# Performance work log

Measured on AMD Instinct MI355X. Metric: run time of the kernel, lower is better.

## Reference

```python
import jax, jax.numpy as jnp
import numpy as np

L = 4          # num_layers
H = 512        # hidden_size == input_size
B, S = 8, 4096
LN_EPS = 1e-5


def parallel_scan_log(coeffs, values):
    """h_t = coeffs_t * h_{t-1} + values_t via Hillis-Steele log-step scan.
    coeffs, values: (B, S, H). Faithful to the torch loop incl. clamp."""
    seq_len = coeffs.shape[1]
    a = jnp.clip(coeffs, 1e-08, 1.0 - 1e-08)
    b = values
    num_steps = int(seq_len - 1).bit_length()
    for step in range(num_steps):
        d = 1 << step
        if d >= seq_len:
            break
        a_prev = jnp.pad(a[:, :-d, :], ((0, 0), (d, 0), (0, 0)), constant_values=1.0)
        b_prev = jnp.pad(b[:, :-d, :], ((0, 0), (d, 0), (0, 0)), constant_values=0.0)
        b = a * b_prev + b   # uses old a (matches a_new/b_new then assign)
        a = a * a_prev
    return b


def mingru_layer(x, Wz, bz, Wh, bh):
    # x: (B,S,in) ; Wz,Wh: (H,in) torch Linear layout (y = x @ W.T + b)
    z = jax.nn.sigmoid(jnp.einsum('bsi,hi->bsh', x, Wz) + bz)
    h_tilde = jnp.tanh(jnp.einsum('bsi,hi->bsh', x, Wh) + bh)
    return parallel_scan_log(1.0 - z, z * h_tilde)


def layer_norm(x, g, b):
    mu = jnp.mean(x, axis=-1, keepdims=True)
    var = jnp.mean(jnp.square(x - mu), axis=-1, keepdims=True)
    return (x - mu) * jax.lax.rsqrt(var + LN_EPS) * g + b


def run_layers(x, Wz, bz, Wh, bh, ln_g, ln_b):
    h = x
    for i in range(L):
        h_new = mingru_layer(h, Wz[i], bz[i], Wh[i], bh[i])
        if i > 0:
            h_new = h_new + h  # residual (shapes match for i>0)
        h = layer_norm(h_new, ln_g, ln_b)  # dropout==Identity (p=0)
    return h


def setup_inputs() -> dict:
    key = jax.random.key(0)
    ks = jax.random.split(key, 12)
    lim = 1.0 / np.sqrt(H)  # torch Linear default init range
    u = lambda k, shp: jax.random.uniform(k, shp, jnp.float32, -lim, lim)
    return {
        'x': jax.random.normal(ks[0], (B, S, H), jnp.float32),
        'Wz_f': u(ks[1], (L, H, H)), 'bz_f': u(ks[2], (L, H)),
        'Wh_f': u(ks[3], (L, H, H)), 'bh_f': u(ks[4], (L, H)),
        'Wz_b': u(ks[5], (L, H, H)), 'bz_b': u(ks[6], (L, H)),
        'Wh_b': u(ks[7], (L, H, H)), 'bh_b': u(ks[8], (L, H)),
        'fusion_w': u(ks[9], (H, 2 * H)), 'fusion_b': u(ks[10], (H,)),
        'ln_g': jnp.ones((H,), jnp.float32), 'ln_b': jnp.zeros((H,), jnp.float32),
    }


def reference(x, Wz_f, bz_f, Wh_f, bh_f, Wz_b, bz_b, Wh_b, bh_b, fusion_w, fusion_b, ln_g, ln_b):
    out_fwd = run_layers(x, Wz_f, bz_f, Wh_f, bh_f, ln_g, ln_b)
    x_rev = jnp.flip(x, axis=1)
    out_bwd = jnp.flip(run_layers(x_rev, Wz_b, bz_b, Wh_b, bh_b, ln_g, ln_b), axis=1)
    out_comb = jnp.concatenate([out_fwd, out_bwd], axis=-1)  # (B,S,2H)
    return jnp.einsum('bsk,hk->bsh', out_comb, fusion_w) + fusion_b
```

## Files before the change

### kernel.cpp

```cpp
#include <hip/hip_runtime.h>

#define HID 512
#define SLEN 4096
#define NB 8
#define BSROWS (NB*SLEN)
#define NLAYER 4
#define CHUNKT 128
#define NCHUNK 32

typedef float f32x4 __attribute__((ext_vector_type(4)));
typedef unsigned int u32x4 __attribute__((ext_vector_type(4)));

__device__ __forceinline__ float bf2f(unsigned short u){
  union { unsigned int i; float f; } v; v.i = ((unsigned int)u) << 16; return v.f;
}
__device__ __forceinline__ unsigned short f2bf(float f){
  union { float f; unsigned int i; } v; v.f = f;
  unsigned int u = v.i;
  u = u + 0x7fffu + ((u >> 16) & 1u);
  return (unsigned short)(u >> 16);
}
__device__ __forceinline__ void mfma_bf16(f32x4& acc, u32x4 a, u32x4 b){
  asm("v_mfma_f32_16x16x32_bf16 %0, %1, %2, %0" : "+v"(acc) : "v"(a), "v"(b));
}
__device__ __forceinline__ void mfma_fence(){
  __builtin_amdgcn_sched_barrier(0);
  asm volatile("s_nop 7\n\ts_nop 7\n\ts_nop 7\n\ts_nop 7");
  __builtin_amdgcn_sched_barrier(0);
}
__device__ __forceinline__ void decode_ab(unsigned int v, float& a, float& b){
  a = (float)(v & 0xffffu) * (1.f/65535.f);
  b = fmaf((float)(v >> 16), 2.f/65535.f, -1.f);
}


__global__ __launch_bounds__(256) void prep_w(
    const float* __restrict__ wzf, const float* __restrict__ whf,
    const float* __restrict__ wzb, const float* __restrict__ whb,
    unsigned short* __restrict__ wbf)
{
  int idx = blockIdx.x*256 + threadIdx.x;
  int i8  = idx & 63;
  int o   = (idx >> 6) & 511;
  int m   = (idx >> 15) & 1;
  int l   = (idx >> 16) & 3;
  int dir = idx >> 18;
  const float* src = dir ? (m ? whb : wzb) : (m ? whf : wzf);
  const float* p = src + ((size_t)(l*512 + o)*512 + i8*8);
  float4 v0 = *(const float4*)p;
  float4 v1 = *(const float4*)(p+4);
  unsigned short* q = wbf + ((((size_t)(dir*4 + l)*2 + m)*512 + o)*512 + i8*8);
  u32x4 outv;
  outv[0] = (unsigned)f2bf(v0.x) | ((unsigned)f2bf(v0.y)<<16);
  outv[1] = (unsigned)f2bf(v0.z) | ((unsigned)f2bf(v0.w)<<16);
  outv[2] = (unsigned)f2bf(v1.x) | ((unsigned)f2bf(v1.y)<<16);
  outv[3] = (unsigned)f2bf(v1.z) | ((unsigned)f2bf(v1.w)<<16);
  *(u32x4*)q = outv;
}

__global__ __launch_bounds__(256) void prep_fw(
    const float* __restrict__ fw, unsigned short* __restrict__ outw)
{
  int idx = blockIdx.x*256 + threadIdx.x;
  const float* p = fw + (size_t)idx*8;
  float4 v0 = *(const float4*)p;
  float4 v1 = *(const float4*)(p+4);
  u32x4 outv;
  outv[0] = (unsigned)f2bf(v0.x) | ((unsigned)f2bf(v0.y)<<16);
  outv[1] = (unsigned)f2bf(v0.z) | ((unsigned)f2bf(v0.w)<<16);
  outv[2] = (unsigned)f2bf(v1.x) | ((unsigned)f2bf(v1.y)<<16);
  outv[3] = (unsigned)f2bf(v1.z) | ((unsigned)f2bf(v1.w)<<16);
  *(u32x4*)(outw + (size_t)idx*8) = outv;
}

__global__ __launch_bounds__(256) void prep_x(
    const float* __restrict__ x, unsigned short* __restrict__ X0)
{
  int idx = blockIdx.x*256 + threadIdx.x;
  int j8  = idx & 63;
  int s   = (idx >> 6) & 4095;
  int b   = (idx >> 18) & 7;
  int dir = idx >> 21;
  int srcs = dir ? (4095 - s) : s;
  const float* p = x + ((size_t)(b*SLEN + srcs)*512 + j8*8);
  float4 v0 = *(const float4*)p;
  float4 v1 = *(const float4*)(p+4);
  u32x4 outv;
  outv[0] = (unsigned)f2bf(v0.x) | ((unsigned)f2bf(v0.y)<<16);
  outv[1] = (unsigned)f2bf(v0.z) | ((unsigned)f2bf(v0.w)<<16);
  outv[2] = (unsigned)f2bf(v1.x) | ((unsigned)f2bf(v1.y)<<16);
  outv[3] = (unsigned)f2bf(v1.z) | ((unsigned)f2bf(v1.w)<<16);
  *(u32x4*)(X0 + ((size_t)((dir*NB + b)*SLEN + s)*512 + j8*8)) = outv;
}


__global__ __launch_bounds__(256) void gate_gemm_scan(
    const unsigned short* __restrict__ X,
    const unsigned short* __restrict__ Wz,
    const unsigned short* __restrict__ Wh,
    const float* __restrict__ bzp, const float* __restrict__ bhp,
    unsigned int* __restrict__ PH,
    float* __restrict__ Aagg, float* __restrict__ Bagg,
    int Mtiles, int CG)
{
  __shared__ __align__(16) unsigned char smem[32768 + 2048];
  unsigned short* As  = (unsigned short*)smem;
  unsigned short* Bzs = (unsigned short*)(smem + 16384);
  unsigned short* Bhs = (unsigned short*)(smem + 24576);
  unsigned int*   SC  = (unsigned int*)smem;
  float* SegP = (float*)(smem + 32768);
  float* SegH = (float*)(smem + 32768 + 1024);

  int hw = blockIdx.x;
  int lg = (hw & 7)*Mtiles + (hw >> 3);
  int nt  = lg & 7;
  int mt  = lg >> 3;

  const int tid = threadIdx.x;
  const int lane = tid & 63;
  const int wv = tid >> 6;
  const int n0 = nt*64;
  const int slot = tid & 7;
  const int rowb = tid >> 3;

  f32x4 accz[2][4], acch[2][4];
  #pragma unroll
  for (int i=0;i<2;++i)
    #pragma unroll
    for (int j=0;j<4;++j){ accz[i][j] = (f32x4)(0.f); acch[i][j] = (f32x4)(0.f); }

  for (int ks=0; ks<8; ++ks){
    int k0 = ks*64;
    #pragma unroll
    for (int it=0; it<4; ++it){
      int row = rowb + it*32;
      u32x4 v = *(const u32x4*)(X + (size_t)(mt*128+row)*512 + k0 + slot*8);
      *(u32x4*)(As + row*64 + ((slot ^ (row&7))<<3)) = v;
    }
    #pragma unroll
    for (int it=0; it<2; ++it){
      int row = rowb + it*32;
      u32x4 vz = *(const u32x4*)(Wz + (size_t)(n0+row)*512 + k0 + slot*8);
      *(u32x4*)(Bzs + row*64 + ((slot ^ (row&7))<<3)) = vz;
      u32x4 vh = *(const u32x4*)(Wh + (size_t)(n0+row)*512 + k0 + slot*8);
      *(u32x4*)(Bhs + row*64 + ((slot ^ (row&7))<<3)) = vh;
    }
    __syncthreads();
    #pragma unroll
    for (int kk=0; kk<2; ++kk){
      int kslot = kk*4 + (lane >> 4);
      u32x4 af[2];
      #pragma unroll
      for (int mf=0; mf<2; ++mf){
        int row = wv*32 + mf*16 + (lane & 15);
        af[mf] = *(const u32x4*)(As + row*64 + ((kslot ^ (row&7))<<3));
      }
      #pragma unroll
      for (int nf=0; nf<4; ++nf){
        int row = nf*16 + (lane & 15);
        u32x4 bz = *(const u32x4*)(Bzs + row*64 + ((kslot ^ (row&7))<<3));
        u32x4 bh = *(const u32x4*)(Bhs + row*64 + ((kslot ^ (row&7))<<3));
        #pragma unroll
        for (int mf=0; mf<2; ++mf){
          mfma_bf16(accz[mf][nf], af[mf], bz);
          mfma_bf16(acch[mf][nf], af[mf], bh);
        }
      }
    }
    __syncthreads();
  }
  mfma_fence();

  #pragma unroll
  for (int nf=0; nf<4; ++nf){
    int colL = nf*16 + (lane & 15);
    float bz = bzp[n0 + colL];
    float bh = bhp[n0 + colL];
    #pragma unroll
    for (int mf=0; mf<2; ++mf){
      int rloc = wv*32 + mf*16 + ((lane>>4)<<2);
      #pragma unroll
      for (int r=0; r<4; ++r){
        float zp = accz[mf][nf][r] + bz;
        float hp = acch[mf][nf][r] + bh;
        float sg = 1.f/(1.f + __expf(-zp));
        float th = 1.f - 2.f/(1.f + __expf(2.f*hp));
        float a = 1.f - sg;
        a = fminf(fmaxf(a, 1e-8f), 1.0f);
        float bv = sg*th;
        unsigned aq = (unsigned)fmaf(a, 65535.f, 0.5f);
        unsigned bq = (unsigned)fmaf(bv, 32767.5f, 32768.0f);
        SC[(rloc + r)*64 + colL] = aq | (bq << 16);
      }
    }
  }
  __syncthreads();

  const int col = tid & 63;
  const int seg = tid >> 6;
  float P = 1.f, Hl = 0.f;
  #pragma unroll
  for (int r=0; r<32; ++r){
    int row = seg*32 + r;
    float a, b; decode_ab(SC[row*64 + col], a, b);
    Hl = fmaf(a, Hl, b);
    P *= a;
    unsigned pq = (unsigned)fmaf(P, 65535.f, 0.5f);
    SC[row*64 + col] = pq | ((unsigned)f2bf(Hl) << 16);
  }
  SegP[seg*64 + col] = P;
  SegH[seg*64 + col] = Hl;
  __syncthreads();

  float Ppre = 1.f, Hpre = 0.f;
  for (int j=0; j<seg; ++j){
    Hpre = fmaf(SegP[j*64 + col], Hpre, SegH[j*64 + col]);
    Ppre *= SegP[j*64 + col];
  }

  const int rowbase = mt*128;
  float Pg = 1.f, Hg = 0.f;
  #pragma unroll
  for (int r=0; r<32; ++r){
    int row = seg*32 + r;
    unsigned v = SC[row*64 + col];
    float Pl = (float)(v & 0xffffu) * (1.f/65535.f);
    float Hlv = bf2f((unsigned short)(v >> 16));
    Pg = Ppre * Pl;
    Hg = fmaf(Pl, Hpre, Hlv);
    unsigned pq = (unsigned)fmaf(Pg, 65535.f, 0.5f);
    PH[(size_t)(rowbase + row)*512 + n0 + col] = pq | ((unsigned)f2bf(Hg) << 16);
  }
  if (seg == 3){
    int chain = (mt >> 5)*512 + n0 + col;
    int c = mt & 31;
    Aagg[c*CG + chain] = Pg;
    Bagg[c*CG + chain] = Hg;
  }
}


__global__ __launch_bounds__(256) void scan_p2(
    const float* __restrict__ Aagg, const float* __restrict__ Bagg,
    float* __restrict__ Hin, int CG)
{
  int chain = blockIdx.x*256 + threadIdx.x;
  float hv = 0.f;
  #pragma unroll
  for (int c=0; c<NCHUNK; ++c){
    Hin[c*CG + chain] = hv;
    hv = fmaf(Aagg[c*CG + chain], hv, Bagg[c*CG + chain]);
  }
}


__global__ __launch_bounds__(256) void recon_ln(
    const unsigned int* __restrict__ PH,
    const float* __restrict__ Hin,
    unsigned short* __restrict__ Xio,
    const float* __restrict__ g, const float* __restrict__ bta,
    int resid, int CG)
{
  int token = blockIdx.x*4 + (threadIdx.x >> 6);
  int lane = threadIdx.x & 63;
  size_t base = (size_t)token*512 + lane*8;
  u32x4 p0 = *(const u32x4*)(PH + base);
  u32x4 p1 = *(const u32x4*)(PH + base + 4);
  int c  = (token >> 7) & 31;
  int bl = token >> 12;
  const float* hin = Hin + (size_t)c*CG + bl*512 + lane*8;
  f32x4 h0 = *(const f32x4*)hin;
  f32x4 h1 = *(const f32x4*)(hin + 4);
  float v[8];
  #pragma unroll
  for (int j=0; j<4; ++j){
    v[j]   = fmaf((float)(p0[j] & 0xffffu)*(1.f/65535.f), h0[j], bf2f((unsigned short)(p0[j] >> 16)));
    v[4+j] = fmaf((float)(p1[j] & 0xffffu)*(1.f/65535.f), h1[j], bf2f((unsigned short)(p1[j] >> 16)));
  }
  if (resid){
    u32x4 xv = *(const u32x4*)(Xio + base);
    #pragma unroll
    for (int w=0; w<4; ++w){
      v[2*w]   += bf2f((unsigned short)(xv[w] & 0xffffu));
      v[2*w+1] += bf2f((unsigned short)(xv[w] >> 16));
    }
  }
  float s = 0.f, s2 = 0.f;
  #pragma unroll
  for (int j=0; j<8; ++j){ s += v[j]; s2 += v[j]*v[j]; }
  #pragma unroll
  for (int o=1; o<64; o<<=1){ s += __shfl_xor(s, o, 64); s2 += __shfl_xor(s2, o, 64); }
  float mu = s * (1.f/512.f);
  float var = s2 * (1.f/512.f) - mu*mu;
  float inv = rsqrtf(var + 1e-5f);
  float4 g0 = *(const float4*)(g + lane*8);
  float4 g1 = *(const float4*)(g + lane*8 + 4);
  float4 b0 = *(const float4*)(bta + lane*8);
  float4 b1 = *(const float4*)(bta + lane*8 + 4);
  float gg[8]  = {g0.x,g0.y,g0.z,g0.w,g1.x,g1.y,g1.z,g1.w};
  float bbv[8] = {b0.x,b0.y,b0.z,b0.w,b1.x,b1.y,b1.z,b1.w};
  u32x4 outv;
  #pragma unroll
  for (int w=0; w<4; ++w){
    float y0 = (v[2*w]   - mu)*inv*gg[2*w]   + bbv[2*w];
    float y1 = (v[2*w+1] - mu)*inv*gg[2*w+1] + bbv[2*w+1];
    outv[w] = (unsigned)f2bf(y0) | ((unsigned)f2bf(y1) << 16);
  }
  *(u32x4*)(Xio + base) = outv;
}


__global__ __launch_bounds__(256) void fusion_gemm(
    const unsigned short* __restrict__ Xf,
    const unsigned short* __restrict__ Wf,
    const float* __restrict__ fb,
    float* __restrict__ outp)
{
  __shared__ __align__(16) unsigned short As[128*64];
  __shared__ __align__(16) unsigned short Bs[64*64];

  int hw = blockIdx.x;
  int lg = (hw & 7)*256 + (hw >> 3);
  int nt = lg & 7;
  int mt = lg >> 3;

  const int tid = threadIdx.x;
  const int lane = tid & 63;
  const int wv = tid >> 6;
  const int n0 = nt*64;
  const int slot = tid & 7;
  const int rowb = tid >> 3;

  f32x4 acc[2][4];
  #pragma unroll
  for (int i=0;i<2;++i)
    #pragma unroll
    for (int j=0;j<4;++j) acc[i][j] = (f32x4)(0.f);

  for (int ks=0; ks<16; ++ks){
    int k0 = ks*64;
    const unsigned short* Abase = Xf + ((k0 >= 512) ? (size_t)BSROWS*512 : 0);
    int kc = k0 & 511;
    #pragma unroll
    for (int it=0; it<4; ++it){
      int row = rowb + it*32;
      int rg = mt*128 + row;
      int sr = (k0 >= 512) ? (rg ^ 4095) : rg;
      u32x4 v = *(const u32x4*)(Abase + (size_t)sr*512 + kc + slot*8);
      *(u32x4*)(As + row*64 + ((slot ^ (row&7))<<3)) = v;
    }
    #pragma unroll
    for (int it=0; it<2; ++it){
      int row = rowb + it*32;
      u32x4 v = *(const u32x4*)(Wf + (size_t)(n0+row)*1024 + k0 + slot*8);
      *(u32x4*)(Bs + row*64 + ((slot ^ (row&7))<<3)) = v;
    }
    __syncthreads();
    #pragma unroll
    for (int kk=0; kk<2; ++kk){
      int kslot = kk*4 + (lane >> 4);
      u32x4 af[2];
      #pragma unroll
      for (int mf=0; mf<2; ++mf){
        int row = wv*32 + mf*16 + (lane & 15);
        af[mf] = *(const u32x4*)(As + row*64 + ((kslot ^ (row&7))<<3));
      }
      #pragma unroll
      for (int nf=0; nf<4; ++nf){
        int row = nf*16 + (lane & 15);
        u32x4 bv = *(const u32x4*)(Bs + row*64 + ((kslot ^ (row&7))<<3));
        #pragma unroll
        for (int mf=0; mf<2; ++mf) mfma_bf16(acc[mf][nf], af[mf], bv);
      }
    }
    __syncthreads();
  }
  mfma_fence();

  #pragma unroll
  for (int nf=0; nf<4; ++nf){
    int col = n0 + nf*16 + (lane & 15);
    float bias = fb[col];
    #pragma unroll
    for (int mf=0; mf<2; ++mf){
      int rb = mt*128 + wv*32 + mf*16 + ((lane>>4)<<2);
      #pragma unroll
      for (int r=0; r<4; ++r)
        outp[(size_t)(rb + r)*512 + col] = acc[mf][nf][r] + bias;
    }
  }
}


extern "C" void kernel_launch(void* const* d_in, const int* in_sizes, int n_in,
                              void* d_out, int out_size, void* d_ws, size_t ws_size,
                              hipStream_t stream)
{
  (void)in_sizes; (void)n_in; (void)out_size;
  const float* x   = (const float*)d_in[0];
  const float* wzf = (const float*)d_in[1];
  const float* bzf = (const float*)d_in[2];
  const float* whf = (const float*)d_in[3];
  const float* bhf = (const float*)d_in[4];
  const float* wzb = (const float*)d_in[5];
  const float* bzb = (const float*)d_in[6];
  const float* whb = (const float*)d_in[7];
  const float* bhb = (const float*)d_in[8];
  const float* fw  = (const float*)d_in[9];
  const float* fbb = (const float*)d_in[10];
  const float* lng = (const float*)d_in[11];
  const float* lnb = (const float*)d_in[12];
  float* outp = (float*)d_out;

  const size_t WbfB = (size_t)16*512*512*2;
  const size_t WfbB = (size_t)512*1024*2;
  const size_t XB   = (size_t)2*BSROWS*512*2;
  const size_t aggB = (size_t)4096*NCHUNK*4;
  int SG = 8;
  for (int c = 1; c <= 8; c <<= 1){
    size_t need = WbfB + WfbB + XB + 3*aggB
                + ((size_t)BSROWS/c)*512*4
                + 1024;
    if (need <= ws_size){ SG = c; break; }
  }
  const int R  = BSROWS / SG;
  const int NBg = NB / SG;
  const int CG = NBg * 512;
  const int Mtiles = R / 128;

  char* ws = (char*)d_ws;
  size_t o = 0;
  unsigned short* Wbf = (unsigned short*)(ws + o); o += WbfB;
  unsigned short* Wfb = (unsigned short*)(ws + o); o += WfbB;
  unsigned short* X   = (unsigned short*)(ws + o); o += XB;
  unsigned int*   PH  = (unsigned int*)  (ws + o); o += (size_t)R*512*4;
  float* Aagg = (float*)(ws + o); o += aggB;
  float* Bagg = (float*)(ws + o); o += aggB;
  float* Hin  = (float*)(ws + o); o += aggB;

  prep_w <<<2048, 256, 0, stream>>>(wzf, whf, wzb, whb, Wbf);
  prep_fw<<<256,  256, 0, stream>>>(fw, Wfb);
  prep_x <<<16384,256, 0, stream>>>(x, X);

  for (int dir = 0; dir < 2; ++dir){
    const float* bz = dir ? bzb : bzf;
    const float* bh = dir ? bhb : bhf;
    for (int g = 0; g < SG; ++g){
      unsigned short* Xg = X + ((size_t)dir*BSROWS + (size_t)g*R)*512;
      for (int l = 0; l < NLAYER; ++l){
        const unsigned short* Wz = Wbf + ((size_t)((dir*4 + l)*2 + 0))*(512*512);
        const unsigned short* Wh = Wbf + ((size_t)((dir*4 + l)*2 + 1))*(512*512);
        gate_gemm_scan<<<Mtiles*8, 256, 0, stream>>>(Xg, Wz, Wh, bz + l*512, bh + l*512,
                                                     PH, Aagg, Bagg, Mtiles, CG);
        scan_p2 <<<CG/256, 256, 0, stream>>>(Aagg, Bagg, Hin, CG);
        recon_ln<<<R/4,    256, 0, stream>>>(PH, Hin, Xg, lng, lnb, l > 0 ? 1 : 0, CG);
      }
    }
  }
  fusion_gemm<<<2048, 256, 0, stream>>>(X, Wfb, fbb, outp);
}
```

Measured before the change: 710.2 us.

## Load GEMM tiles directly to LDS via global_load_lds and swizzle scan buffer

Replaces register-staged global loads plus LDS stores in both the gate GEMM and the fusion GEMM with the direct global-to-LDS load instruction. The XOR swizzle moves from the store address to the global source address, so the LDS layout stays the same while the rows are read in permuted order. It also adds an XOR swizzle to the packed scan scratch indexing to reduce LDS bank conflicts during the column-wise scan. Both aim to cut VGPR traffic, instruction count and LDS conflicts, at the risk of relying on correct per-wave contiguous destination semantics and on synchronization still being correct without explicit vmcnt waits.

```diff
diff --git a/kernel.cpp b/kernel.cpp
--- a/kernel.cpp
+++ b/kernel.cpp
@@ -11,6 +11,9 @@
 typedef float f32x4 __attribute__((ext_vector_type(4)));
 typedef unsigned int u32x4 __attribute__((ext_vector_type(4)));
 
+typedef const __attribute__((address_space(1))) unsigned int* gas_u32p;
+typedef __attribute__((address_space(3))) unsigned int* las_u32p;
+
 __device__ __forceinline__ float bf2f(unsigned short u){
   union { unsigned int i; float f; } v; v.i = ((unsigned int)u) << 16; return v.f;
 }
@@ -31,6 +34,12 @@
 __device__ __forceinline__ void decode_ab(unsigned int v, float& a, float& b){
   a = (float)(v & 0xffffu) * (1.f/65535.f);
   b = fmaf((float)(v >> 16), 2.f/65535.f, -1.f);
+}
+__device__ __forceinline__ void gload_lds16(const unsigned short* g, unsigned short* l){
+  __builtin_amdgcn_global_load_lds((gas_u32p)(const void*)g, (las_u32p)(void*)l, 16, 0, 0);
+}
+__device__ __forceinline__ int scidx(int row, int col){
+  return row*64 + (col ^ (((row>>2)&3)<<4));
 }
 
 
@@ -120,8 +129,8 @@
   const int lane = tid & 63;
   const int wv = tid >> 6;
   const int n0 = nt*64;
-  const int slot = tid & 7;
-  const int rowb = tid >> 3;
+  const int lrow  = lane >> 3;
+  const int slotp = (lane & 7) ^ (lrow & 7);
 
   f32x4 accz[2][4], acch[2][4];
   #pragma unroll
@@ -133,17 +142,17 @@
     int k0 = ks*64;
     #pragma unroll
     for (int it=0; it<4; ++it){
-      int row = rowb + it*32;
-      u32x4 v = *(const u32x4*)(X + (size_t)(mt*128+row)*512 + k0 + slot*8);
-      *(u32x4*)(As + row*64 + ((slot ^ (row&7))<<3)) = v;
+      int row = it*32 + wv*8 + lrow;
+      gload_lds16(X + (size_t)(mt*128 + row)*512 + k0 + slotp*8,
+                  As + (it*32 + wv*8)*64);
     }
     #pragma unroll
     for (int it=0; it<2; ++it){
-      int row = rowb + it*32;
-      u32x4 vz = *(const u32x4*)(Wz + (size_t)(n0+row)*512 + k0 + slot*8);
-      *(u32x4*)(Bzs + row*64 + ((slot ^ (row&7))<<3)) = vz;
-      u32x4 vh = *(const u32x4*)(Wh + (size_t)(n0+row)*512 + k0 + slot*8);
-      *(u32x4*)(Bhs + row*64 + ((slot ^ (row&7))<<3)) = vh;
+      int row = it*32 + wv*8 + lrow;
+      gload_lds16(Wz + (size_t)(n0 + row)*512 + k0 + slotp*8,
+                  Bzs + (it*32 + wv*8)*64);
+      gload_lds16(Wh + (size_t)(n0 + row)*512 + k0 + slotp*8,
+                  Bhs + (it*32 + wv*8)*64);
     }
     __syncthreads();
     #pragma unroll
@@ -190,7 +199,7 @@
         float bv = sg*th;
         unsigned aq = (unsigned)fmaf(a, 65535.f, 0.5f);
         unsigned bq = (unsigned)fmaf(bv, 32767.5f, 32768.0f);
-        SC[(rloc + r)*64 + colL] = aq | (bq << 16);
+        SC[scidx(rloc + r, colL)] = aq | (bq << 16);
       }
     }
   }
@@ -202,11 +211,11 @@
   #pragma unroll
   for (int r=0; r<32; ++r){
     int row = seg*32 + r;
-    float a, b; decode_ab(SC[row*64 + col], a, b);
+    float a, b; decode_ab(SC[scidx(row, col)], a, b);
     Hl = fmaf(a, Hl, b);
     P *= a;
     unsigned pq = (unsigned)fmaf(P, 65535.f, 0.5f);
-    SC[row*64 + col] = pq | ((unsigned)f2bf(Hl) << 16);
+    SC[scidx(row, col)] = pq | ((unsigned)f2bf(Hl) << 16);
   }
   SegP[seg*64 + col] = P;
   SegH[seg*64 + col] = Hl;
@@ -223,7 +232,7 @@
   #pragma unroll
   for (int r=0; r<32; ++r){
     int row = seg*32 + r;
-    unsigned v = SC[row*64 + col];
+    unsigned v = SC[scidx(row, col)];
     float Pl = (float)(v & 0xffffu) * (1.f/65535.f);
     float Hlv = bf2f((unsigned short)(v >> 16));
     Pg = Ppre * Pl;
@@ -328,8 +337,8 @@
   const int lane = tid & 63;
   const int wv = tid >> 6;
   const int n0 = nt*64;
-  const int slot = tid & 7;
-  const int rowb = tid >> 3;
+  const int lrow  = lane >> 3;
+  const int slotp = (lane & 7) ^ (lrow & 7);
 
   f32x4 acc[2][4];
   #pragma unroll
@@ -341,19 +350,19 @@
     int k0 = ks*64;
     const unsigned short* Abase = Xf + ((k0 >= 512) ? (size_t)BSROWS*512 : 0);
     int kc = k0 & 511;
+    int flip = (k0 >= 512) ? 4095 : 0;
     #pragma unroll
     for (int it=0; it<4; ++it){
-      int row = rowb + it*32;
-      int rg = mt*128 + row;
-      int sr = (k0 >= 512) ? (rg ^ 4095) : rg;
-      u32x4 v = *(const u32x4*)(Abase + (size_t)sr*512 + kc + slot*8);
-      *(u32x4*)(As + row*64 + ((slot ^ (row&7))<<3)) = v;
+      int row = it*32 + wv*8 + lrow;
+      int sr = (mt*128 + row) ^ flip;
+      gload_lds16(Abase + (size_t)sr*512 + kc + slotp*8,
+                  As + (it*32 + wv*8)*64);
     }
     #pragma unroll
     for (int it=0; it<2; ++it){
-      int row = rowb + it*32;
-      u32x4 v = *(const u32x4*)(Wf + (size_t)(n0+row)*1024 + k0 + slot*8);
-      *(u32x4*)(Bs + row*64 + ((slot ^ (row&7))<<3)) = v;
+      int row = it*32 + wv*8 + lrow;
+      gload_lds16(Wf + (size_t)(n0 + row)*1024 + k0 + slotp*8,
+                  Bs + (it*32 + wv*8)*64);
     }
     __syncthreads();
     #pragma unroll
```

Measured after the change: 736.3 us. +3.7%, slower.
